# Performance work log

Measured on AMD Instinct MI355X. Metric: run time of the kernel, lower is better.

## Reference

```python
import jax, jax.numpy as jnp
import numpy as np

B, C, H, W = 8, 256, 128, 128
WS = 8   # window size
NH = 8   # num heads
NEG = -1e9


def _rel_coords_table(ws):
    # continuous relative coords table, shape [1, 2ws-1, 2ws-1, 2]
    r = np.arange(-(ws - 1), ws, dtype=np.float32)
    t = np.stack(np.meshgrid(r, r, indexing='ij'), axis=-1)[None]
    t = t / (ws - 1) * 8.0
    t = np.sign(t) * np.log2(np.abs(t) + 1.0) / np.log2(8.0)
    return jnp.asarray(t, dtype=jnp.float32)


def _rel_pos_index(ws):
    coords = np.stack(np.meshgrid(np.arange(ws), np.arange(ws), indexing='ij'))  # [2,ws,ws]
    flat = coords.reshape(2, -1)
    rel = (flat[:, :, None] - flat[:, None, :]).transpose(1, 2, 0).astype(np.int64)  # [N,N,2]
    rel[..., 0] += ws - 1
    rel[..., 1] += ws - 1
    rel[..., 0] *= 2 * ws - 1
    return jnp.asarray(rel.sum(-1))  # [N,N]


def setup_inputs() -> dict:
    key = jax.random.key(0)
    ks = jax.random.split(key, 10)
    d8 = C // 8
    return {
        'x': jax.random.normal(ks[0], (B, C, H, W), jnp.float32),
        'y': jax.random.normal(ks[1], (B, C, H, W), jnp.float32),
        'Wq': jax.random.normal(ks[2], (d8, C), jnp.float32) * 0.02,
        'bq': jnp.zeros((d8,), jnp.float32),
        'Wk': jax.random.normal(ks[3], (d8, C), jnp.float32) * 0.02,
        'bk': jnp.zeros((d8,), jnp.float32),
        'Wv': jax.random.normal(ks[4], (C, C), jnp.float32) * 0.02,
        'bv': jnp.zeros((C,), jnp.float32),
        'gamma': jnp.full((1,), 0.5, jnp.float32),
        'qkv_w': jax.random.normal(ks[5], (3 * C, C), jnp.float32) * 0.02,
        'q_bias': jnp.zeros((C,), jnp.float32),
        'v_bias': jnp.zeros((C,), jnp.float32),
        'logit_scale': jnp.log(10.0 * jnp.ones((NH, 1, 1), jnp.float32)),
        'cpb_w1': jax.random.normal(ks[6], (512, 2), jnp.float32) * 0.02,
        'cpb_b1': jnp.zeros((512,), jnp.float32),
        'cpb_w2': jax.random.normal(ks[7], (NH, 512), jnp.float32) * 0.02,
        'proj_w': jax.random.normal(ks[8], (C, C), jnp.float32) * 0.02,
        'proj_b': jnp.zeros((C,), jnp.float32),
    }


def _criss_cross(x, y, Wq, bq, Wk, bk, Wv, bv, gamma):
    # 1x1 convs as einsum channel projections
    q = jnp.einsum('bchw,oc->bohw', x, Wq) + bq[None, :, None, None]
    k = jnp.einsum('bchw,oc->bohw', x, Wk) + bk[None, :, None, None]
    v = jnp.einsum('bchw,oc->bohw', y, Wv) + bv[None, :, None, None]
    h = x.shape[2]
    # column (H-axis) attention with -inf on diagonal; row (W-axis) attention
    diag = jnp.where(jnp.eye(h, dtype=bool), NEG, 0.0).astype(x.dtype)  # [H,H]
    eH = jnp.einsum('bchw,bcgw->bhwg', q, k) + diag[None, :, None, :]   # [B,H,W,H]
    eW = jnp.einsum('bchw,bchv->bhwv', q, k)                            # [B,H,W,W]
    att = jax.nn.softmax(jnp.concatenate([eH, eW], axis=3), axis=3)
    aH, aW = att[..., :h], att[..., h:]
    oH = jnp.einsum('bhwg,bcgw->bchw', aH, v)
    oW = jnp.einsum('bhwv,bchv->bchw', aW, v)
    return gamma[0] * (oH + oW) + x


def _window_attention(xw, qkv_w, q_bias, v_bias, logit_scale,
                      cpb_w1, cpb_b1, cpb_w2, proj_w, proj_b):
    B_, N, Cc = xw.shape
    hd = Cc // NH
    bias = jnp.concatenate([q_bias, jnp.zeros_like(v_bias), v_bias])
    qkv = (xw @ qkv_w.T + bias).reshape(B_, N, 3, NH, hd).transpose(2, 0, 3, 1, 4)
    q, k, v = qkv[0], qkv[1], qkv[2]  # [B_, NH, N, hd]
    qn = q / jnp.maximum(jnp.linalg.norm(q, axis=-1, keepdims=True), 1e-12)
    kn = k / jnp.maximum(jnp.linalg.norm(k, axis=-1, keepdims=True), 1e-12)
    scale = jnp.exp(jnp.minimum(logit_scale, jnp.log(jnp.float32(100.0))))  # [NH,1,1]
    attn = jnp.einsum('bhnd,bhmd->bhnm', qn, kn) * scale[None]
    # continuous relative position bias via inline MLP
    tbl = jax.nn.relu(_rel_coords_table(WS) @ cpb_w1.T + cpb_b1) @ cpb_w2.T  # [1,2ws-1,2ws-1,NH]
    tbl = tbl.reshape(-1, NH)
    rpb = tbl[_rel_pos_index(WS).reshape(-1)].reshape(N, N, NH).transpose(2, 0, 1)
    attn = jax.nn.softmax(attn + (16.0 * jax.nn.sigmoid(rpb))[None], axis=-1)
    out = jnp.einsum('bhnm,bhmd->bnhd', attn, v).reshape(B_, N, Cc)
    return out @ proj_w.T + proj_b


def reference(x, y, Wq, bq, Wk, bk, Wv, bv, gamma,
              qkv_w, q_bias, v_bias, logit_scale,
              cpb_w1, cpb_b1, cpb_w2, proj_w, proj_b):
    cc = _criss_cross(x, y, Wq, bq, Wk, bk, Wv, bv, gamma)   # [B,C,H,W]
    xh = cc.transpose(0, 2, 3, 1)                            # [B,H,W,C]
    win = xh.reshape(B, H // WS, WS, W // WS, WS, C)
    win = win.transpose(0, 1, 3, 2, 4, 5).reshape(-1, WS * WS, C)
    wa = _window_attention(win, qkv_w, q_bias, v_bias, logit_scale,
                           cpb_w1, cpb_b1, cpb_w2, proj_w, proj_b)
    out = wa.reshape(B, H // WS, W // WS, WS, WS, C)
    out = out.transpose(0, 1, 3, 2, 4, 5).reshape(B, H, W, C)
    return out.transpose(0, 3, 1, 2)                         # [B,C,H,W]
```

## Files before the change

### kernel.cpp

```cpp
#include <hip/hip_runtime.h>
#include <cstdio>
#include <cstddef>
#include <cstdint>

#define F_B 8
#define F_C 256
#define F_H 128
#define F_W 128
#define F_HW 16384

typedef __attribute__((ext_vector_type(8))) short short8;
typedef __attribute__((ext_vector_type(4))) short short4v;
typedef __attribute__((ext_vector_type(4))) float float4v;

__device__ __forceinline__ float wred_sum(float v) {
#pragma unroll
  for (int o = 1; o < 64; o <<= 1) v += __shfl_xor(v, o);
  return v;
}

__device__ __forceinline__ unsigned short f2bf(float f) {
  union {
    float f;
    uint32_t u;
  } v;
  v.f = f;
  return (unsigned short)((v.u + 0x7fffu + ((v.u >> 16) & 1u)) >> 16);
}

__device__ __forceinline__ float bf2f(unsigned short u) {
  union {
    uint32_t u;
    float f;
  } v;
  v.u = ((uint32_t)u) << 16;
  return v.f;
}

__device__ __forceinline__ void async_copy16(const unsigned short* g, unsigned short* l) {
  __builtin_amdgcn_global_load_lds((const __attribute__((address_space(1))) void*)g,
                                   (__attribute__((address_space(3))) void*)l, 16, 0, 0);
}

__global__ void build_aux2(const float* __restrict__ Wq, const float* __restrict__ Wk,
                           const float* __restrict__ bq, const float* __restrict__ bk,
                           const float* __restrict__ q_bias, const float* __restrict__ v_bias,
                           const float* __restrict__ Wv, const float* __restrict__ qkv_w,
                           const float* __restrict__ proj_w, unsigned short* __restrict__ qk_wb,
                           float* __restrict__ qk_b, float* __restrict__ qkv_b,
                           unsigned short* __restrict__ Wvb, unsigned short* __restrict__ qkv_wb,
                           unsigned short* __restrict__ proj_wb) {
  int t = blockIdx.x * 256 + threadIdx.x;
  if (t < 8192) {
    qk_wb[t] = f2bf(Wq[t]);
    qk_wb[8192 + t] = f2bf(Wk[t]);
  }
  if (t < 65536) {
    Wvb[t] = f2bf(Wv[t]);
    proj_wb[t] = f2bf(proj_w[t]);
  }
  if (t < 196608) qkv_wb[t] = f2bf(qkv_w[t]);
  if (t < 32) {
    qk_b[t] = bq[t];
    qk_b[32 + t] = bk[t];
  }
  if (t < 256) {
    qkv_b[t] = q_bias[t];
    qkv_b[256 + t] = 0.0f;
    qkv_b[512 + t] = v_bias[t];
  }
}

__device__ __forceinline__ float cpb_coord(int a) {
  float v = (float)(a - 7) * (8.0f / 7.0f);
  float lg = log2f(fabsf(v) + 1.0f) * (1.0f / 3.0f);
  return (v < 0.0f) ? -lg : lg;
}

__global__ void cpb_table(const float* __restrict__ w1, const float* __restrict__ b1,
                          const float* __restrict__ w2, float* __restrict__ tblS) {
  int e = blockIdx.x;
  int yi = e / 15, xi = e % 15;
  float ry = cpb_coord(yi), rx = cpb_coord(xi);
  __shared__ float hid[512];
  int t = threadIdx.x;
  for (int j = t; j < 512; j += 256) {
    float hv = w1[j * 2] * ry + w1[j * 2 + 1] * rx + b1[j];
    hid[j] = fmaxf(hv, 0.0f);
  }
  __syncthreads();
  if (t < 8) {
    float s = 0.0f;
    for (int j = 0; j < 512; j++) s += hid[j] * w2[t * 512 + j];
    tblS[e * 8 + t] = 16.0f / (1.0f + __expf(-s));
  }
}

__global__ void build_rpbt(const float* __restrict__ tblS, float* __restrict__ rpbt) {
  int t = blockIdx.x * 256 + threadIdx.x;
  int h = t >> 12, i = (t >> 6) & 63, j = t & 63;
  int e = ((i >> 3) - (j >> 3) + 7) * 15 + ((i & 7) - (j & 7) + 7);
  rpbt[t] = tblS[e * 8 + h];
}

__global__ void transpose_x(const float* __restrict__ in, float* __restrict__ outf,
                            unsigned short* __restrict__ outb) {
  __shared__ float tile[32][33];
  int b = blockIdx.z;
  int p0 = blockIdx.x * 32;
  int c0 = blockIdx.y * 32;
  const float* src = in + (size_t)b * F_C * F_HW;
  int tx = threadIdx.x, ty = threadIdx.y;
#pragma unroll
  for (int i = 0; i < 4; i++) {
    tile[ty + i * 8][tx] = src[(size_t)(c0 + ty + i * 8) * F_HW + p0 + tx];
  }
  __syncthreads();
#pragma unroll
  for (int i = 0; i < 4; i++) {
    size_t idx = (size_t)b * F_HW * F_C + (size_t)(p0 + ty + i * 8) * F_C + c0 + tx;
    float v = tile[tx][ty + i * 8];
    outf[idx] = v;
    outb[idx] = f2bf(v);
  }
}

__global__ void transpose_y(const float* __restrict__ in, unsigned short* __restrict__ outb) {
  __shared__ float tile[32][33];
  int b = blockIdx.z;
  int p0 = blockIdx.x * 32;
  int c0 = blockIdx.y * 32;
  const float* src = in + (size_t)b * F_C * F_HW;
  int tx = threadIdx.x, ty = threadIdx.y;
#pragma unroll
  for (int i = 0; i < 4; i++) {
    tile[ty + i * 8][tx] = src[(size_t)(c0 + ty + i * 8) * F_HW + p0 + tx];
  }
  __syncthreads();
#pragma unroll
  for (int i = 0; i < 4; i++) {
    size_t idx = (size_t)b * F_HW * F_C + (size_t)(p0 + ty + i * 8) * F_C + c0 + tx;
    outb[idx] = f2bf(tile[tx][ty + i * 8]);
  }
}

template <int BN, int OUT>
__global__ __launch_bounds__(256) void gemm_mfma(const unsigned short* __restrict__ A,
                                                 const unsigned short* __restrict__ Wt,
                                                 const float* __restrict__ bias, void* Cmat,
                                                 int M, int N) {
  constexpr int WN = BN / 2;
  constexpr int NREP = WN / 16;
  __shared__ __align__(16) unsigned short As[128 * 32];
  __shared__ __align__(16) unsigned short Bs[BN * 32];
  int m0 = blockIdx.y * 128;
  int n0 = blockIdx.x * BN;
  int t = threadIdx.x;
  int wid = t >> 6, lane = t & 63;
  int wr = wid >> 1, wc = wid & 1;

  float4v acc[4][NREP] = {};

  for (int k0 = 0; k0 < 256; k0 += 32) {
    __syncthreads();
#pragma unroll
    for (int j = 0; j < 2; j++) {
      int r = wid * 32 + j * 16 + (lane >> 2);
      int kg = (lane & 3) ^ (r & 3);
      const unsigned short* gp = A + (size_t)(m0 + r) * 256 + k0 + kg * 8;
      async_copy16(gp, As + (wid * 32 + j * 16) * 32);
    }
#pragma unroll
    for (int j = 0; j < BN / 64; j++) {
      int r = wid * (BN / 4) + j * 16 + (lane >> 2);
      int kg = (lane & 3) ^ (r & 3);
      const unsigned short* gp = Wt + (size_t)(n0 + r) * 256 + k0 + kg * 8;
      async_copy16(gp, Bs + (wid * (BN / 4) + j * 16) * 32);
    }
    __syncthreads();
    short8 af[4];
#pragma unroll
    for (int mi = 0; mi < 4; mi++) {
      int row = wr * 64 + mi * 16 + (lane & 15);
      int kg = (lane >> 4) ^ (row & 3);
      af[mi] = *(const short8*)(As + row * 32 + kg * 8);
    }
    short8 bfr[NREP];
#pragma unroll
    for (int ni = 0; ni < NREP; ni++) {
      int col = wc * WN + ni * 16 + (lane & 15);
      int kg = (lane >> 4) ^ (col & 3);
      bfr[ni] = *(const short8*)(Bs + col * 32 + kg * 8);
    }
#pragma unroll
    for (int mi = 0; mi < 4; mi++)
#pragma unroll
      for (int ni = 0; ni < NREP; ni++)
        acc[mi][ni] =
            __builtin_amdgcn_mfma_f32_16x16x32_bf16(af[mi], bfr[ni], acc[mi][ni], 0, 0, 0);
  }
#pragma unroll
  for (int ni = 0; ni < NREP; ni++) {
    int col = n0 + wc * WN + ni * 16 + (lane & 15);
    float bn = bias[col];
#pragma unroll
    for (int mi = 0; mi < 4; mi++) {
      int row0 = m0 + wr * 64 + mi * 16 + (lane >> 4) * 4;
#pragma unroll
      for (int r = 0; r < 4; r++) {
        float v = acc[mi][ni][r] + bn;
        int row = row0 + r;
        if (OUT == 0) {
          ((float*)Cmat)[(size_t)row * N + col] = v;
        } else if (OUT == 1) {
          int bb = row >> 14, p = row & 16383;
          ((float*)Cmat)[((size_t)bb * N + col) * F_HW + p] = v;
        } else {
          ((unsigned short*)Cmat)[(size_t)row * N + col] = f2bf(v);
        }
      }
    }
  }
}

template <int MODE>
__global__ __launch_bounds__(256) void cc_logits(const float* __restrict__ qk,
                                                 unsigned short* __restrict__ e) {
  int x = blockIdx.x;
  int b = blockIdx.y;
  size_t base = (size_t)b * F_HW;
  __shared__ float kt[32][132];
  int t = threadIdx.x;
  {
    int gk = t >> 1, c0 = (t & 1) * 16;
    size_t krow = (MODE == 0) ? ((size_t)gk * F_W + x) : ((size_t)x * F_W + gk);
    const float4* src = (const float4*)(qk + (base + krow) * 64 + 32 + c0);
#pragma unroll
    for (int q4 = 0; q4 < 4; q4++) {
      float4 v = src[q4];
      kt[c0 + q4 * 4 + 0][gk] = v.x;
      kt[c0 + q4 * 4 + 1][gk] = v.y;
      kt[c0 + q4 * 4 + 2][gk] = v.z;
      kt[c0 + q4 * 4 + 3][gk] = v.w;
    }
  }
  __syncthreads();
  int i = t >> 1, g0 = (t & 1) * 64;
  size_t qrow = (MODE == 0) ? ((size_t)i * F_W + x) : ((size_t)x * F_W + i);
  const float4* qp = (const float4*)(qk + (base + qrow) * 64);
  float qreg[32];
#pragma unroll
  for (int q4 = 0; q4 < 8; q4++) {
    float4 v = qp[q4];
    qreg[q4 * 4 + 0] = v.x;
    qreg[q4 * 4 + 1] = v.y;
    qreg[q4 * 4 + 2] = v.z;
    qreg[q4 * 4 + 3] = v.w;
  }
  float acc[64];
#pragma unroll
  for (int g = 0; g < 64; g++) acc[g] = 0.0f;
  for (int c = 0; c < 32; c++) {
    float qv = qreg[c];
#pragma unroll
    for (int g = 0; g < 64; g++) acc[g] += qv * kt[c][g0 + g];
  }
  if (MODE == 0) {
    int d = i - g0;
    if (d >= 0 && d < 64) acc[d] = -1e9f;
  }
  unsigned short* ep = e + (base + qrow) * 256 + MODE * 128 + g0;
#pragma unroll
  for (int g = 0; g < 64; g += 8) {
    short8 pk;
#pragma unroll
    for (int j = 0; j < 8; j++) pk[j] = (short)f2bf(__expf(acc[g + j]));
    *(short8*)(ep + g) = pk;
  }
}

__global__ __launch_bounds__(256) void cc_sums(const unsigned short* __restrict__ e,
                                               float* __restrict__ rsum) {
  int wave = (blockIdx.x * 256 + threadIdx.x) >> 6;
  int lane = threadIdx.x & 63;
  short4v v = *(const short4v*)(e + (size_t)wave * 256 + lane * 4);
  float s = bf2f((unsigned short)v[0]) + bf2f((unsigned short)v[1]) +
            bf2f((unsigned short)v[2]) + bf2f((unsigned short)v[3]);
  s = wred_sum(s);
  if (lane == 0) rsum[wave] = 1.0f / s;
}

template <int MODE>
__global__ __launch_bounds__(256) void cc_pv_mfma(const unsigned short* __restrict__ eb,
                                                  const unsigned short* __restrict__ vtb,
                                                  const float* __restrict__ rsum,
                                                  const float* __restrict__ gamma,
                                                  const float* __restrict__ xt,
                                                  float* __restrict__ po,
                                                  unsigned short* __restrict__ ccb) {
  int x = blockIdx.x, b = blockIdx.y;
  size_t base = (size_t)b * F_HW;
  __shared__ __align__(16) unsigned short As[128 * 128];
  __shared__ __align__(16) unsigned short Vs[256 * 64];
  int t = threadIdx.x;
  int wid = t >> 6, lane = t & 63;
  int wr = wid >> 1, wc = wid & 1;
  {
    int i = t >> 1, half = t & 1;
    size_t pix = (MODE == 0) ? ((size_t)i * F_W + x) : ((size_t)x * F_W + i);
    float rv = rsum[base + pix];
    const unsigned short* ep = eb + (base + pix) * 256 + MODE * 128 + half * 64;
    int g = ((i >> 3) & 7) ^ (i & 7);
#pragma unroll
    for (int s = 0; s < 8; s++) {
      short8 vin = *(const short8*)(ep + s * 8);
      short8 vo;
#pragma unroll
      for (int j = 0; j < 8; j++) vo[j] = (short)f2bf(bf2f((unsigned short)vin[j]) * rv);
      int slot = (half * 8 + s) ^ g;
      *(short8*)(As + i * 128 + slot * 8) = vo;
    }
  }
  float4v acc[4][8] = {};
#pragma unroll
  for (int kc = 0; kc < 2; kc++) {
    __syncthreads();
    {
      int ko = t >> 5, cj = t & 31;
      short8 rowv[8];
#pragma unroll
      for (int r = 0; r < 8; r++) {
        int kk = kc * 64 + ko * 8 + r;
        size_t pixk = (MODE == 0) ? ((size_t)kk * F_W + x) : ((size_t)x * F_W + kk);
        rowv[r] = *(const short8*)(vtb + (base + pixk) * 256 + cj * 8);
      }
#pragma unroll
      for (int j = 0; j < 8; j++) {
        short8 col;
#pragma unroll
        for (int r = 0; r < 8; r++) col[r] = rowv[r][j];
        int c = cj * 8 + j;
        int slot = ko ^ ((c >> 3) & 7) ^ (c & 7);
        *(short8*)(Vs + c * 64 + slot * 8) = col;
      }
    }
    __syncthreads();
#pragma unroll
    for (int ksub = 0; ksub < 2; ksub++) {
      short8 af[4];
#pragma unroll
      for (int mi = 0; mi < 4; mi++) {
        int i = wr * 64 + mi * 16 + (lane & 15);
        int slot = (kc * 8 + ksub * 4 + (lane >> 4)) ^ ((i >> 3) & 7) ^ (i & 7);
        af[mi] = *(const short8*)(As + i * 128 + slot * 8);
      }
      short8 bfv[8];
#pragma unroll
      for (int ni = 0; ni < 8; ni++) {
        int c = wc * 128 + ni * 16 + (lane & 15);
        int slot = (ksub * 4 + (lane >> 4)) ^ ((c >> 3) & 7) ^ (c & 7);
        bfv[ni] = *(const short8*)(Vs + c * 64 + slot * 8);
      }
#pragma unroll
      for (int mi = 0; mi < 4; mi++)
#pragma unroll
        for (int ni = 0; ni < 8; ni++)
          acc[mi][ni] =
              __builtin_amdgcn_mfma_f32_16x16x32_bf16(af[mi], bfv[ni], acc[mi][ni], 0, 0, 0);
    }
  }
  float gm = gamma[0];
#pragma unroll
  for (int mi = 0; mi < 4; mi++) {
#pragma unroll
    for (int ni = 0; ni < 8; ni++) {
#pragma unroll
      for (int r = 0; r < 4; r++) {
        int i = wr * 64 + mi * 16 + (lane >> 4) * 4 + r;
        int c = wc * 128 + ni * 16 + (lane & 15);
        size_t pix = (MODE == 0) ? ((size_t)i * F_W + x) : ((size_t)x * F_W + i);
        size_t idx = (base + pix) * 256 + c;
        if (MODE == 0) {
          po[idx] = acc[mi][ni][r];
        } else {
          float v = gm * (po[idx] + acc[mi][ni][r]) + xt[idx];
          ccb[idx] = f2bf(v);
        }
      }
    }
  }
}

__global__ __launch_bounds__(256) void win_attn_mfma(const unsigned short* __restrict__ qkv,
                                                     const float* __restrict__ logit_scale,
                                                     const float* __restrict__ rpbt,
                                                     unsigned short* __restrict__ out) {
  __shared__ __align__(16) unsigned short Pl[4][4096];
  __shared__ __align__(16) unsigned short Vt[4][2048];
  int win = blockIdx.x;
  int wid = threadIdx.x >> 6, lane = threadIdx.x & 63;
  int hh = blockIdx.y * 4 + wid;
  int b = win >> 8, wy = (win >> 4) & 15, wx = win & 15;
  size_t pbase = (size_t)b * F_HW + (size_t)(wy * 8) * F_W + wx * 8;
  int il = lane & 15, kg = lane >> 4;

  short8 qb[4], ka[4];
#pragma unroll
  for (int ni = 0; ni < 4; ni++) {
    int i = ni * 16 + il;
    size_t row = (pbase + (size_t)(i >> 3) * F_W + (i & 7)) * 768 + hh * 32 + kg * 8;
    short8 qv = *(const short8*)(qkv + row);
    short8 kv = *(const short8*)(qkv + row + 256);
    float qss = 0.0f, kss = 0.0f;
#pragma unroll
    for (int j = 0; j < 8; j++) {
      float qf = bf2f((unsigned short)qv[j]);
      float kf = bf2f((unsigned short)kv[j]);
      qss += qf * qf;
      kss += kf * kf;
    }
    qss += __shfl_xor(qss, 16);
    qss += __shfl_xor(qss, 32);
    kss += __shfl_xor(kss, 16);
    kss += __shfl_xor(kss, 32);
    float qinv = 1.0f / fmaxf(sqrtf(qss), 1e-12f);
    float kinv = 1.0f / fmaxf(sqrtf(kss), 1e-12f);
#pragma unroll
    for (int j = 0; j < 8; j++) {
      qb[ni][j] = (short)f2bf(bf2f((unsigned short)qv[j]) * qinv);
      ka[ni][j] = (short)f2bf(bf2f((unsigned short)kv[j]) * kinv);
    }
  }

  if (lane < 32) {
    int jb = lane >> 2, db = lane & 3;
    short8 rows[8];
#pragma unroll
    for (int r = 0; r < 8; r++) {
      rows[r] =
          *(const short8*)(qkv + (pbase + (size_t)jb * F_W + r) * 768 + hh * 32 + 512 + db * 8);
    }
#pragma unroll
    for (int c = 0; c < 8; c++) {
      int d = db * 8 + c;
      short8 col;
#pragma unroll
      for (int r = 0; r < 8; r++) col[r] = rows[r][c];
      *(short8*)(Vt[wid] + d * 64 + ((jb ^ (d & 7)) * 8)) = col;
    }
  }

  float4v sacc[4][4] = {};
#pragma unroll
  for (int mj = 0; mj < 4; mj++)
#pragma unroll
    for (int ni = 0; ni < 4; ni++)
      sacc[mj][ni] = __builtin_amdgcn_mfma_f32_16x16x32_bf16(ka[mj], qb[ni], sacc[mj][ni], 0, 0, 0);

  float scale = __expf(fminf(logit_scale[hh], 4.605170185988091f));

#pragma unroll
  for (int ni = 0; ni < 4; ni++) {
    int i = ni * 16 + il;
    const float* rp = rpbt + ((size_t)hh * 64 + i) * 64;
    float sv[16];
    float mx = -1e30f;
#pragma unroll
    for (int mj = 0; mj < 4; mj++) {
      float4 rb = *(const float4*)(rp + mj * 16 + kg * 4);
      float rbs[4] = {rb.x, rb.y, rb.z, rb.w};
#pragma unroll
      for (int r = 0; r < 4; r++) {
        float v = sacc[mj][ni][r] * scale + rbs[r];
        sv[mj * 4 + r] = v;
        mx = fmaxf(mx, v);
      }
    }
    mx = fmaxf(mx, __shfl_xor(mx, 16));
    mx = fmaxf(mx, __shfl_xor(mx, 32));
    float sm = 0.0f;
#pragma unroll
    for (int u = 0; u < 16; u++) {
      sv[u] = __expf(sv[u] - mx);
      sm += sv[u];
    }
    sm += __shfl_xor(sm, 16);
    sm += __shfl_xor(sm, 32);
    float inv = 1.0f / sm;
#pragma unroll
    for (int mj = 0; mj < 4; mj++) {
      int j0 = mj * 16 + kg * 4;
      short4v pk;
#pragma unroll
      for (int r = 0; r < 4; r++) pk[r] = (short)f2bf(sv[mj * 4 + r] * inv);
      int byteoff = i * 128 + (((j0 >> 3) ^ (i & 7)) * 16) + (j0 & 7) * 2;
      *(short4v*)((char*)Pl[wid] + byteoff) = pk;
    }
  }
  __syncthreads();

  float4v oacc[2][4] = {};
#pragma unroll
  for (int kc = 0; kc < 2; kc++) {
    short8 va[2];
#pragma unroll
    for (int md = 0; md < 2; md++) {
      int d = md * 16 + il;
      va[md] = *(const short8*)((char*)Vt[wid] + d * 128 + (((kc * 4 + kg) ^ (d & 7)) * 16));
    }
    short8 pb[4];
#pragma unroll
    for (int ni = 0; ni < 4; ni++) {
      int i = ni * 16 + il;
      pb[ni] = *(const short8*)((char*)Pl[wid] + i * 128 + (((kc * 4 + kg) ^ (i & 7)) * 16));
    }
#pragma unroll
    for (int md = 0; md < 2; md++)
#pragma unroll
      for (int ni = 0; ni < 4; ni++)
        oacc[md][ni] =
            __builtin_amdgcn_mfma_f32_16x16x32_bf16(va[md], pb[ni], oacc[md][ni], 0, 0, 0);
  }

#pragma unroll
  for (int ni = 0; ni < 4; ni++) {
    int i = ni * 16 + il;
    size_t orow = (pbase + (size_t)(i >> 3) * F_W + (i & 7)) * 256 + hh * 32;
#pragma unroll
    for (int md = 0; md < 2; md++) {
      int d0 = md * 16 + kg * 4;
      short4v pk;
#pragma unroll
      for (int r = 0; r < 4; r++) pk[r] = (short)f2bf(oacc[md][ni][r]);
      *(short4v*)(out + orow + d0) = pk;
    }
  }
}

extern "C" void kernel_launch(void* const* d_in, const int* in_sizes, int n_in,
                              void* d_out, int out_size, void* d_ws, size_t ws_size,
                              hipStream_t stream) {
  const float* x = (const float*)d_in[0];
  const float* y = (const float*)d_in[1];
  const float* Wq = (const float*)d_in[2];
  const float* bq = (const float*)d_in[3];
  const float* Wk = (const float*)d_in[4];
  const float* bk = (const float*)d_in[5];
  const float* Wv = (const float*)d_in[6];
  const float* bv = (const float*)d_in[7];
  const float* gamma = (const float*)d_in[8];
  const float* qkv_w = (const float*)d_in[9];
  const float* q_bias = (const float*)d_in[10];
  const float* v_bias = (const float*)d_in[11];
  const float* logit_scale = (const float*)d_in[12];
  const float* cpb_w1 = (const float*)d_in[13];
  const float* cpb_b1 = (const float*)d_in[14];
  const float* cpb_w2 = (const float*)d_in[15];
  const float* proj_w = (const float*)d_in[16];
  const float* proj_b = (const float*)d_in[17];

  float* ws = (float*)d_ws;
  const size_t NPX = (size_t)F_B * F_HW;
  const size_t M1 = NPX * 256;
  size_t f_xt = 0;
  size_t f_eb = M1;
  size_t f_vtb = M1 + M1 / 2;
  size_t f_po = 2 * M1;
  size_t f_ccb = 3 * M1;
  size_t f_qkb = 3 * M1 + M1 / 2;
  size_t f_wts = f_qkb + NPX * 64;
  size_t o_qkwb = f_wts;
  size_t o_Wvb = o_qkwb + 8192;
  size_t o_qkvwb = o_Wvb + 32768;
  size_t o_projwb = o_qkvwb + 98304;
  size_t o_qkb2 = o_projwb + 32768;
  size_t o_qkvb2 = o_qkb2 + 64;
  size_t o_tbl = o_qkvb2 + 768;
  size_t o_rsum = o_tbl + 1800;
  size_t o_rpbt = o_rsum + NPX;
  size_t need = (o_rpbt + 32768) * sizeof(float);
  if (ws_size < need) {
    fprintf(stderr, "kernel_launch: ws too small: %zu < %zu\n", ws_size, need);
    return;
  }
  float* xt = ws + f_xt;
  unsigned short* qkvb = (unsigned short*)(ws + f_xt);
  unsigned short* ytb = (unsigned short*)(ws + f_eb);
  unsigned short* eb = (unsigned short*)(ws + f_eb);
  unsigned short* xb = (unsigned short*)(ws + f_vtb);
  unsigned short* vtb = (unsigned short*)(ws + f_vtb);
  float* po = ws + f_po;
  unsigned short* attn_b = (unsigned short*)(ws + f_po);
  unsigned short* ccb = (unsigned short*)(ws + f_ccb);
  float* qkb = ws + f_qkb;
  unsigned short* qk_wb = (unsigned short*)(ws + o_qkwb);
  unsigned short* Wvb = (unsigned short*)(ws + o_Wvb);
  unsigned short* qkv_wb = (unsigned short*)(ws + o_qkvwb);
  unsigned short* proj_wb = (unsigned short*)(ws + o_projwb);
  float* qk_b = ws + o_qkb2;
  float* qkv_b = ws + o_qkvb2;
  float* tblS = ws + o_tbl;
  float* rsum = ws + o_rsum;
  float* rpbt = ws + o_rpbt;

  build_aux2<<<dim3(768), dim3(256), 0, stream>>>(Wq, Wk, bq, bk, q_bias, v_bias, Wv, qkv_w,
                                                  proj_w, qk_wb, qk_b, qkv_b, Wvb, qkv_wb,
                                                  proj_wb);
  cpb_table<<<dim3(225), dim3(256), 0, stream>>>(cpb_w1, cpb_b1, cpb_w2, tblS);
  build_rpbt<<<dim3(128), dim3(256), 0, stream>>>(tblS, rpbt);
  transpose_x<<<dim3(512, 8, 8), dim3(32, 8), 0, stream>>>(x, xt, xb);
  transpose_y<<<dim3(512, 8, 8), dim3(32, 8), 0, stream>>>(y, ytb);
  gemm_mfma<64, 0><<<dim3(1, 1024), dim3(256), 0, stream>>>(xb, qk_wb, qk_b, qkb, (int)NPX,
                                                            64);
  gemm_mfma<128, 2><<<dim3(2, 1024), dim3(256), 0, stream>>>(ytb, Wvb, bv, vtb, (int)NPX, 256);
  cc_logits<0><<<dim3(128, 8), dim3(256), 0, stream>>>(qkb, eb);
  cc_logits<1><<<dim3(128, 8), dim3(256), 0, stream>>>(qkb, eb);
  cc_sums<<<dim3(32768), dim3(256), 0, stream>>>(eb, rsum);
  cc_pv_mfma<0><<<dim3(128, 8), dim3(256), 0, stream>>>(eb, vtb, rsum, gamma, xt, po, ccb);
  cc_pv_mfma<1><<<dim3(128, 8), dim3(256), 0, stream>>>(eb, vtb, rsum, gamma, xt, po, ccb);
  gemm_mfma<128, 2><<<dim3(6, 1024), dim3(256), 0, stream>>>(ccb, qkv_wb, qkv_b, qkvb,
                                                             (int)NPX, 768);
  win_attn_mfma<<<dim3(2048, 2), dim3(256), 0, stream>>>(qkvb, logit_scale, rpbt, attn_b);
  gemm_mfma<128, 1><<<dim3(2, 1024), dim3(256), 0, stream>>>(attn_b, proj_wb, proj_b, d_out,
                                                             (int)NPX, 256);
}
```

Measured before the change: 700.7 us.

## Fuse softmax row sums into logits, drop fp32 intermediates, swizzle GEMM grid

Row sums of the exponentiated logits are now accumulated inside cc_logits (one partial per direction) rather than in a separate cc_sums pass that re-read the whole bf16 energy buffer. The fp32 transposed x copy and fp32 partial output are replaced by bf16 buffers, cutting memory traffic in the transpose and PV kernels. GEMM launches switch to a 1D grid with an XCD-style swizzle to improve cache locality across the chip's dies. Sums now come from unrounded fp32 exps rather than the stored bf16 values, and the residual and partial use bf16 precision, which adds rounding error.

```diff
diff --git a/kernel.cpp b/kernel.cpp
--- a/kernel.cpp
+++ b/kernel.cpp
@@ -12,12 +12,6 @@
 typedef __attribute__((ext_vector_type(8))) short short8;
 typedef __attribute__((ext_vector_type(4))) short short4v;
 typedef __attribute__((ext_vector_type(4))) float float4v;
-
-__device__ __forceinline__ float wred_sum(float v) {
-#pragma unroll
-  for (int o = 1; o < 64; o <<= 1) v += __shfl_xor(v, o);
-  return v;
-}
 
 __device__ __forceinline__ unsigned short f2bf(float f) {
   union {
@@ -103,8 +97,7 @@
   rpbt[t] = tblS[e * 8 + h];
 }
 
-__global__ void transpose_x(const float* __restrict__ in, float* __restrict__ outf,
-                            unsigned short* __restrict__ outb) {
+__global__ void transpose_bf(const float* __restrict__ in, unsigned short* __restrict__ outb) {
   __shared__ float tile[32][33];
   int b = blockIdx.z;
   int p0 = blockIdx.x * 32;
@@ -119,27 +112,6 @@
 #pragma unroll
   for (int i = 0; i < 4; i++) {
     size_t idx = (size_t)b * F_HW * F_C + (size_t)(p0 + ty + i * 8) * F_C + c0 + tx;
-    float v = tile[tx][ty + i * 8];
-    outf[idx] = v;
-    outb[idx] = f2bf(v);
-  }
-}
-
-__global__ void transpose_y(const float* __restrict__ in, unsigned short* __restrict__ outb) {
-  __shared__ float tile[32][33];
-  int b = blockIdx.z;
-  int p0 = blockIdx.x * 32;
-  int c0 = blockIdx.y * 32;
-  const float* src = in + (size_t)b * F_C * F_HW;
-  int tx = threadIdx.x, ty = threadIdx.y;
-#pragma unroll
-  for (int i = 0; i < 4; i++) {
-    tile[ty + i * 8][tx] = src[(size_t)(c0 + ty + i * 8) * F_HW + p0 + tx];
-  }
-  __syncthreads();
-#pragma unroll
-  for (int i = 0; i < 4; i++) {
-    size_t idx = (size_t)b * F_HW * F_C + (size_t)(p0 + ty + i * 8) * F_C + c0 + tx;
     outb[idx] = f2bf(tile[tx][ty + i * 8]);
   }
 }
@@ -148,13 +120,19 @@
 __global__ __launch_bounds__(256) void gemm_mfma(const unsigned short* __restrict__ A,
                                                  const unsigned short* __restrict__ Wt,
                                                  const float* __restrict__ bias, void* Cmat,
-                                                 int M, int N) {
+                                                 int M, int N, int gx) {
   constexpr int WN = BN / 2;
   constexpr int NREP = WN / 16;
   __shared__ __align__(16) unsigned short As[128 * 32];
   __shared__ __align__(16) unsigned short Bs[BN * 32];
-  int m0 = blockIdx.y * 128;
-  int n0 = blockIdx.x * BN;
+  int nwg = gridDim.x;
+  int id = blockIdx.x;
+  int cpx = nwg >> 3;
+  int swz = (id & 7) * cpx + (id >> 3);
+  int by = swz / gx;
+  int bx = swz - by * gx;
+  int m0 = by * 128;
+  int n0 = bx * BN;
   int t = threadIdx.x;
   int wid = t >> 6, lane = t & 63;
   int wr = wid >> 1, wc = wid & 1;
@@ -225,7 +203,8 @@
 
 template <int MODE>
 __global__ __launch_bounds__(256) void cc_logits(const float* __restrict__ qk,
-                                                 unsigned short* __restrict__ e) {
+                                                 unsigned short* __restrict__ e,
+                                                 float* __restrict__ sums) {
   int x = blockIdx.x;
   int b = blockIdx.y;
   size_t base = (size_t)b * F_HW;
@@ -270,33 +249,30 @@
     if (d >= 0 && d < 64) acc[d] = -1e9f;
   }
   unsigned short* ep = e + (base + qrow) * 256 + MODE * 128 + g0;
+  float s = 0.0f;
 #pragma unroll
   for (int g = 0; g < 64; g += 8) {
     short8 pk;
 #pragma unroll
-    for (int j = 0; j < 8; j++) pk[j] = (short)f2bf(__expf(acc[g + j]));
+    for (int j = 0; j < 8; j++) {
+      float ev = __expf(acc[g + j]);
+      s += ev;
+      pk[j] = (short)f2bf(ev);
+    }
     *(short8*)(ep + g) = pk;
   }
-}
-
-__global__ __launch_bounds__(256) void cc_sums(const unsigned short* __restrict__ e,
-                                               float* __restrict__ rsum) {
-  int wave = (blockIdx.x * 256 + threadIdx.x) >> 6;
-  int lane = threadIdx.x & 63;
-  short4v v = *(const short4v*)(e + (size_t)wave * 256 + lane * 4);
-  float s = bf2f((unsigned short)v[0]) + bf2f((unsigned short)v[1]) +
-            bf2f((unsigned short)v[2]) + bf2f((unsigned short)v[3]);
-  s = wred_sum(s);
-  if (lane == 0) rsum[wave] = 1.0f / s;
+  s += __shfl_xor(s, 1);
+  if ((t & 1) == 0) sums[base + qrow] = s;
 }
 
 template <int MODE>
 __global__ __launch_bounds__(256) void cc_pv_mfma(const unsigned short* __restrict__ eb,
                                                   const unsigned short* __restrict__ vtb,
-                                                  const float* __restrict__ rsum,
+                                                  const float* __restrict__ sumH,
+                                                  const float* __restrict__ sumW,
                                                   const float* __restrict__ gamma,
-                                                  const float* __restrict__ xt,
-                                                  float* __restrict__ po,
+                                                  const unsigned short* __restrict__ xb,
+                                                  unsigned short* __restrict__ pob,
                                                   unsigned short* __restrict__ ccb) {
   int x = blockIdx.x, b = blockIdx.y;
   size_t base = (size_t)b * F_HW;
@@ -308,7 +284,7 @@
   {
     int i = t >> 1, half = t & 1;
     size_t pix = (MODE == 0) ? ((size_t)i * F_W + x) : ((size_t)x * F_W + i);
-    float rv = rsum[base + pix];
+    float rv = 1.0f / (sumH[base + pix] + sumW[base + pix]);
     const unsigned short* ep = eb + (base + pix) * 256 + MODE * 128 + half * 64;
     int g = ((i >> 3) & 7) ^ (i & 7);
 #pragma unroll
@@ -381,9 +357,9 @@
         size_t pix = (MODE == 0) ? ((size_t)i * F_W + x) : ((size_t)x * F_W + i);
         size_t idx = (base + pix) * 256 + c;
         if (MODE == 0) {
-          po[idx] = acc[mi][ni][r];
+          pob[idx] = f2bf(acc[mi][ni][r]);
         } else {
-          float v = gm * (po[idx] + acc[mi][ni][r]) + xt[idx];
+          float v = gm * (bf2f(pob[idx]) + acc[mi][ni][r]) + bf2f(xb[idx]);
           ccb[idx] = f2bf(v);
         }
       }
@@ -562,12 +538,12 @@
   float* ws = (float*)d_ws;
   const size_t NPX = (size_t)F_B * F_HW;
   const size_t M1 = NPX * 256;
-  size_t f_xt = 0;
-  size_t f_eb = M1;
-  size_t f_vtb = M1 + M1 / 2;
-  size_t f_po = 2 * M1;
-  size_t f_ccb = 3 * M1;
-  size_t f_qkb = 3 * M1 + M1 / 2;
+  size_t f_xb = 0;
+  size_t f_ytb = M1 / 2;
+  size_t f_vtb = M1;
+  size_t f_pob = M1 + M1 / 2;
+  size_t f_ccb = 2 * M1;
+  size_t f_qkb = 2 * M1 + M1 / 2;
   size_t f_wts = f_qkb + NPX * 64;
   size_t o_qkwb = f_wts;
   size_t o_Wvb = o_qkwb + 8192;
@@ -576,21 +552,21 @@
   size_t o_qkb2 = o_projwb + 32768;
   size_t o_qkvb2 = o_qkb2 + 64;
   size_t o_tbl = o_qkvb2 + 768;
-  size_t o_rsum = o_tbl + 1800;
-  size_t o_rpbt = o_rsum + NPX;
+  size_t o_sumH = o_tbl + 1800;
+  size_t o_sumW = o_sumH + NPX;
+  size_t o_rpbt = o_sumW + NPX;
   size_t need = (o_rpbt + 32768) * sizeof(float);
   if (ws_size < need) {
     fprintf(stderr, "kernel_launch: ws too small: %zu < %zu\n", ws_size, need);
     return;
   }
-  float* xt = ws + f_xt;
-  unsigned short* qkvb = (unsigned short*)(ws + f_xt);
-  unsigned short* ytb = (unsigned short*)(ws + f_eb);
-  unsigned short* eb = (unsigned short*)(ws + f_eb);
-  unsigned short* xb = (unsigned short*)(ws + f_vtb);
+  unsigned short* xb = (unsigned short*)(ws + f_xb);
+  unsigned short* qkvb = (unsigned short*)(ws + f_xb);
+  unsigned short* ytb = (unsigned short*)(ws + f_ytb);
+  unsigned short* eb = (unsigned short*)(ws + f_ytb);
   unsigned short* vtb = (unsigned short*)(ws + f_vtb);
-  float* po = ws + f_po;
-  unsigned short* attn_b = (unsigned short*)(ws + f_po);
+  unsigned short* pob = (unsigned short*)(ws + f_pob);
+  unsigned short* attn_b = (unsigned short*)(ws + f_pob);
   unsigned short* ccb = (unsigned short*)(ws + f_ccb);
   float* qkb = ws + f_qkb;
   unsigned short* qk_wb = (unsigned short*)(ws + o_qkwb);
@@ -600,7 +576,8 @@
   float* qk_b = ws + o_qkb2;
   float* qkv_b = ws + o_qkvb2;
   float* tblS = ws + o_tbl;
-  float* rsum = ws + o_rsum;
+  float* sumH = ws + o_sumH;
+  float* sumW = ws + o_sumW;
   float* rpbt = ws + o_rpbt;
 
   build_aux2<<<dim3(768), dim3(256), 0, stream>>>(Wq, Wk, bq, bk, q_bias, v_bias, Wv, qkv_w,
@@ -608,19 +585,20 @@
                                                   proj_wb);
   cpb_table<<<dim3(225), dim3(256), 0, stream>>>(cpb_w1, cpb_b1, cpb_w2, tblS);
   build_rpbt<<<dim3(128), dim3(256), 0, stream>>>(tblS, rpbt);
-  transpose_x<<<dim3(512, 8, 8), dim3(32, 8), 0, stream>>>(x, xt, xb);
-  transpose_y<<<dim3(512, 8, 8), dim3(32, 8), 0, stream>>>(y, ytb);
-  gemm_mfma<64, 0><<<dim3(1, 1024), dim3(256), 0, stream>>>(xb, qk_wb, qk_b, qkb, (int)NPX,
-                                                            64);
-  gemm_mfma<128, 2><<<dim3(2, 1024), dim3(256), 0, stream>>>(ytb, Wvb, bv, vtb, (int)NPX, 256);
-  cc_logits<0><<<dim3(128, 8), dim3(256), 0, stream>>>(qkb, eb);
-  cc_logits<1><<<dim3(128, 8), dim3(256), 0, stream>>>(qkb, eb);
-  cc_sums<<<dim3(32768), dim3(256), 0, stream>>>(eb, rsum);
-  cc_pv_mfma<0><<<dim3(128, 8), dim3(256), 0, stream>>>(eb, vtb, rsum, gamma, xt, po, ccb);
-  cc_pv_mfma<1><<<dim3(128, 8), dim3(256), 0, stream>>>(eb, vtb, rsum, gamma, xt, po, ccb);
-  gemm_mfma<128, 2><<<dim3(6, 1024), dim3(256), 0, stream>>>(ccb, qkv_wb, qkv_b, qkvb,
-                                                             (int)NPX, 768);
+  transpose_bf<<<dim3(512, 8, 8), dim3(32, 8), 0, stream>>>(x, xb);
+  transpose_bf<<<dim3(512, 8, 8), dim3(32, 8), 0, stream>>>(y, ytb);
+  gemm_mfma<64, 0><<<dim3(1024), dim3(256), 0, stream>>>(xb, qk_wb, qk_b, qkb, (int)NPX, 64,
+                                                         1);
+  gemm_mfma<128, 2><<<dim3(2048), dim3(256), 0, stream>>>(ytb, Wvb, bv, vtb, (int)NPX, 256, 2);
+  cc_logits<0><<<dim3(128, 8), dim3(256), 0, stream>>>(qkb, eb, sumH);
+  cc_logits<1><<<dim3(128, 8), dim3(256), 0, stream>>>(qkb, eb, sumW);
+  cc_pv_mfma<0><<<dim3(128, 8), dim3(256), 0, stream>>>(eb, vtb, sumH, sumW, gamma, xb, pob,
+                                                        ccb);
+  cc_pv_mfma<1><<<dim3(128, 8), dim3(256), 0, stream>>>(eb, vtb, sumH, sumW, gamma, xb, pob,
+                                                        ccb);
+  gemm_mfma<128, 2><<<dim3(6144), dim3(256), 0, stream>>>(ccb, qkv_wb, qkv_b, qkvb, (int)NPX,
+                                                          768, 6);
   win_attn_mfma<<<dim3(2048, 2), dim3(256), 0, stream>>>(qkvb, logit_scale, rpbt, attn_b);
-  gemm_mfma<128, 1><<<dim3(2, 1024), dim3(256), 0, stream>>>(attn_b, proj_wb, proj_b, d_out,
-                                                             (int)NPX, 256);
-}
+  gemm_mfma<128, 1><<<dim3(2048), dim3(256), 0, stream>>>(attn_b, proj_wb, proj_b, d_out,
+                                                          (int)NPX, 256, 2);
+}
```

Result: faster. 618.8 us (-11.7%).
